# Performance work log

Hardware: AMD Instinct MI355X
Metric: run time of the kernel (lower is better)

Reference implementation:

```python
import jax, jax.numpy as jnp
import numpy as np

TEMPERATURE = 2.0
N, C = 16384, 1000


def _margin(x, targets):
    """Per-row: top1 - top2 if the target class attains the max, else 0."""
    top2 = jax.lax.top_k(x, 2)[0]                                  # [N, 2]
    tval = jnp.take_along_axis(x, targets[:, None], axis=1)[:, 0]  # [N]
    return jnp.where(tval == top2[:, 0], top2[:, 0] - top2[:, 1], jnp.zeros((), x.dtype))


def setup_inputs() -> dict:
    key = jax.random.key(0)
    ks = jax.random.split(key, 8)
    outs = {f"outputs{i+1}": jax.random.normal(ks[i], (N, C), dtype=jnp.float32) for i in range(6)}
    outs["mimic"] = jax.random.normal(ks[6], (N, C), dtype=jnp.float32)
    outs["targets"] = jax.random.randint(ks[7], (N,), 0, C)
    outs["n_test"] = N
    return outs


def reference(outputs1, outputs2, outputs3, outputs4, outputs5, outputs6, mimic, targets, n_test):
    t = targets[:n_test]
    heads = [outputs1, outputs2, outputs3, outputs4, outputs5, outputs6, mimic]
    # [n_test, 7] stacked margins (d1..d6, m) in original ordering
    margins = jnp.stack([_margin(h[:n_test], t) for h in heads], axis=1)
    out_threshold = jax.nn.softmax(margins / TEMPERATURE, axis=1)
    max_preds = jnp.max(jnp.stack([outputs1, outputs2, outputs3, outputs4, outputs5, outputs6]))
    return max_preds, out_threshold
```

## Files before the change

kernel.cpp:

```cpp
#include <hip/hip_runtime.h>
#include <math.h>


__global__ __launch_bounds__(256) void margin_kernel(
    const float* __restrict__ h0, const float* __restrict__ h1,
    const float* __restrict__ h2, const float* __restrict__ h3,
    const float* __restrict__ h4, const float* __restrict__ h5,
    const float* __restrict__ h6,
    const int* __restrict__ targets,
    float* __restrict__ margins,
    float* __restrict__ partials,
    int N, int C)
{
    const int lane = threadIdx.x & 63;
    const int waveInBlock = threadIdx.x >> 6;
    const int p = blockIdx.x * 4 + waveInBlock;
    const int head = p / N;
    const int row  = p - head * N;

    const float* base;
    switch (head) {
        case 0: base = h0; break;
        case 1: base = h1; break;
        case 2: base = h2; break;
        case 3: base = h3; break;
        case 4: base = h4; break;
        case 5: base = h5; break;
        default: base = h6; break;
    }
    base += (size_t)row * C;

    const float4* v = (const float4*)base;
    const int nvec = C >> 2;
    float m1 = -INFINITY, m2 = -INFINITY;
    #pragma unroll
    for (int it = 0; it < 4; ++it) {
        int idx = it * 64 + lane;
        if (idx < nvec) {
            float4 x = v[idx];
            float vals[4] = {x.x, x.y, x.z, x.w};
            #pragma unroll
            for (int k = 0; k < 4; ++k) {
                float val = vals[k];
                if (val > m1) { m2 = m1; m1 = val; }
                else if (val > m2) { m2 = val; }
            }
        }
    }
    #pragma unroll
    for (int off = 32; off >= 1; off >>= 1) {
        float o1 = __shfl_xor(m1, off);
        float o2 = __shfl_xor(m2, off);
        float hi = fmaxf(m1, o1);
        float lo = fminf(m1, o1);
        m2 = fmaxf(lo, fmaxf(m2, o2));
        m1 = hi;
    }

    __shared__ float smax[4];
    if (lane == 0) {
        int t = targets[row];
        float tval = base[t];
        float margin = (tval == m1) ? (m1 - m2) : 0.0f;
        margins[head * N + row] = margin;
        smax[waveInBlock] = (head < 6) ? m1 : -INFINITY;
    }
    __syncthreads();
    if (threadIdx.x == 0) {
        float bm = fmaxf(fmaxf(smax[0], smax[1]), fmaxf(smax[2], smax[3]));
        partials[blockIdx.x] = bm;
    }
}

__global__ __launch_bounds__(1024) void reduce_max_kernel(
    const float* __restrict__ partials, int n, float* __restrict__ out)
{
    float m = -INFINITY;
    for (int i = threadIdx.x; i < n; i += 1024) m = fmaxf(m, partials[i]);
    #pragma unroll
    for (int off = 32; off >= 1; off >>= 1) m = fmaxf(m, __shfl_xor(m, off));
    __shared__ float s[16];
    int lane = threadIdx.x & 63, w = threadIdx.x >> 6;
    if (lane == 0) s[w] = m;
    __syncthreads();
    if (threadIdx.x == 0) {
        float r = -INFINITY;
        #pragma unroll
        for (int i = 0; i < 16; ++i) r = fmaxf(r, s[i]);
        out[0] = r;
    }
}

__global__ __launch_bounds__(256) void softmax_kernel(
    const float* __restrict__ margins, float* __restrict__ out, int N)
{
    int row = blockIdx.x * blockDim.x + threadIdx.x;
    if (row >= N) return;
    float m[7];
    float mx = -INFINITY;
    #pragma unroll
    for (int j = 0; j < 7; ++j) { m[j] = margins[j * N + row]; mx = fmaxf(mx, m[j]); }
    float s = 0.0f;
    #pragma unroll
    for (int j = 0; j < 7; ++j) { m[j] = expf((m[j] - mx) * 0.5f); s += m[j]; }
    float inv = 1.0f / s;
    #pragma unroll
    for (int j = 0; j < 7; ++j) out[row * 7 + j] = m[j] * inv;
}

extern "C" void kernel_launch(void* const* d_in, const int* in_sizes, int n_in,
                              void* d_out, int out_size, void* d_ws, size_t ws_size,
                              hipStream_t stream) {
    const float* h0 = (const float*)d_in[0];
    const float* h1 = (const float*)d_in[1];
    const float* h2 = (const float*)d_in[2];
    const float* h3 = (const float*)d_in[3];
    const float* h4 = (const float*)d_in[4];
    const float* h5 = (const float*)d_in[5];
    const float* h6 = (const float*)d_in[6];
    const int* targets = (const int*)d_in[7];

    const int N = in_sizes[7];
    const int C = in_sizes[0] / N;

    float* margins  = (float*)d_ws;
    float* partials = margins + 7 * N;
    const int pairs  = 7 * N;
    const int nblocks = pairs / 4;

    margin_kernel<<<nblocks, 256, 0, stream>>>(h0, h1, h2, h3, h4, h5, h6,
                                               targets, margins, partials, N, C);
    reduce_max_kernel<<<1, 1024, 0, stream>>>(partials, nblocks, (float*)d_out);
    softmax_kernel<<<(N + 255) / 256, 256, 0, stream>>>(margins, (float*)d_out + 1, N);
}
```

Measured before the change: 391.1 us.

## Process two rows per wave, use branchless top-2, and merge reduce with softmax

Each wave now handles two rows, and all float4 loads are issued up front, which raises memory-level parallelism. The branchy top-2 update is replaced with fmin/fmax arithmetic. The grid becomes 2D with the head index taken from blockIdx.y, which removes the integer division. The separate max-reduce and softmax kernels are merged into one epilogue launch to save a kernel launch. The code assumes N is divisible by 8 and C is in the range where three full float4 sweeps are valid (at least 768).

```diff
diff --git a/kernel.cpp b/kernel.cpp
--- a/kernel.cpp
+++ b/kernel.cpp
@@ -1,6 +1,10 @@
 #include <hip/hip_runtime.h>
 #include <math.h>
 
+
+#define WAVES_PER_BLOCK 4
+#define ROWS_PER_WAVE 2
+#define ROWS_PER_BLOCK (WAVES_PER_BLOCK * ROWS_PER_WAVE)
 
 __global__ __launch_bounds__(256) void margin_kernel(
     const float* __restrict__ h0, const float* __restrict__ h1,
@@ -14,9 +18,7 @@
 {
     const int lane = threadIdx.x & 63;
     const int waveInBlock = threadIdx.x >> 6;
-    const int p = blockIdx.x * 4 + waveInBlock;
-    const int head = p / N;
-    const int row  = p - head * N;
+    const int head = blockIdx.y;
 
     const float* base;
     switch (head) {
@@ -28,73 +30,91 @@
         case 5: base = h5; break;
         default: base = h6; break;
     }
-    base += (size_t)row * C;
 
-    const float4* v = (const float4*)base;
+    const int row0 = (blockIdx.x * WAVES_PER_BLOCK + waveInBlock) * ROWS_PER_WAVE;
+    const int row1 = row0 + 1;
+    const float* b0 = base + (size_t)row0 * C;
+    const float* b1 = base + (size_t)row1 * C;
+    const float4* v0 = (const float4*)b0;
+    const float4* v1 = (const float4*)b1;
     const int nvec = C >> 2;
-    float m1 = -INFINITY, m2 = -INFINITY;
+
+    float4 a0 = v0[lane];
+    float4 a1 = v0[64 + lane];
+    float4 a2 = v0[128 + lane];
+    float4 c0 = v1[lane];
+    float4 c1 = v1[64 + lane];
+    float4 c2 = v1[128 + lane];
+    float4 a3 = make_float4(-INFINITY, -INFINITY, -INFINITY, -INFINITY);
+    float4 c3 = a3;
+    if (192 + lane < nvec) {
+        a3 = v0[192 + lane];
+        c3 = v1[192 + lane];
+    }
+
+    float m1a = -INFINITY, m2a = -INFINITY;
+    float m1c = -INFINITY, m2c = -INFINITY;
+    float va[16] = {a0.x,a0.y,a0.z,a0.w, a1.x,a1.y,a1.z,a1.w,
+                    a2.x,a2.y,a2.z,a2.w, a3.x,a3.y,a3.z,a3.w};
+    float vc[16] = {c0.x,c0.y,c0.z,c0.w, c1.x,c1.y,c1.z,c1.w,
+                    c2.x,c2.y,c2.z,c2.w, c3.x,c3.y,c3.z,c3.w};
     #pragma unroll
-    for (int it = 0; it < 4; ++it) {
-        int idx = it * 64 + lane;
-        if (idx < nvec) {
-            float4 x = v[idx];
-            float vals[4] = {x.x, x.y, x.z, x.w};
-            #pragma unroll
-            for (int k = 0; k < 4; ++k) {
-                float val = vals[k];
-                if (val > m1) { m2 = m1; m1 = val; }
-                else if (val > m2) { m2 = val; }
-            }
-        }
+    for (int k = 0; k < 16; ++k) {
+        float x = va[k];
+        m2a = fmaxf(m2a, fminf(m1a, x));
+        m1a = fmaxf(m1a, x);
+        float y = vc[k];
+        m2c = fmaxf(m2c, fminf(m1c, y));
+        m1c = fmaxf(m1c, y);
     }
+
     #pragma unroll
     for (int off = 32; off >= 1; off >>= 1) {
-        float o1 = __shfl_xor(m1, off);
-        float o2 = __shfl_xor(m2, off);
-        float hi = fmaxf(m1, o1);
-        float lo = fminf(m1, o1);
-        m2 = fmaxf(lo, fmaxf(m2, o2));
-        m1 = hi;
+        float o1a = __shfl_xor(m1a, off);
+        float o2a = __shfl_xor(m2a, off);
+        float o1c = __shfl_xor(m1c, off);
+        float o2c = __shfl_xor(m2c, off);
+        m2a = fmaxf(fmaxf(m2a, o2a), fminf(m1a, o1a));
+        m1a = fmaxf(m1a, o1a);
+        m2c = fmaxf(fmaxf(m2c, o2c), fminf(m1c, o1c));
+        m1c = fmaxf(m1c, o1c);
     }
 
-    __shared__ float smax[4];
+    __shared__ float smax[WAVES_PER_BLOCK];
     if (lane == 0) {
-        int t = targets[row];
-        float tval = base[t];
-        float margin = (tval == m1) ? (m1 - m2) : 0.0f;
-        margins[head * N + row] = margin;
-        smax[waveInBlock] = (head < 6) ? m1 : -INFINITY;
+        int t0 = targets[row0];
+        int t1 = targets[row1];
+        float tv0 = b0[t0];
+        float tv1 = b1[t1];
+        margins[head * N + row0] = (tv0 == m1a) ? (m1a - m2a) : 0.0f;
+        margins[head * N + row1] = (tv1 == m1c) ? (m1c - m2c) : 0.0f;
+        smax[waveInBlock] = fmaxf(m1a, m1c);
     }
     __syncthreads();
-    if (threadIdx.x == 0) {
+    if (threadIdx.x == 0 && head < 6) {
         float bm = fmaxf(fmaxf(smax[0], smax[1]), fmaxf(smax[2], smax[3]));
-        partials[blockIdx.x] = bm;
+        partials[head * gridDim.x + blockIdx.x] = bm;
     }
 }
 
-__global__ __launch_bounds__(1024) void reduce_max_kernel(
-    const float* __restrict__ partials, int n, float* __restrict__ out)
+__global__ __launch_bounds__(256) void epilogue_kernel(
+    const float* __restrict__ margins, const float* __restrict__ partials,
+    int npart, float* __restrict__ out, int N)
 {
-    float m = -INFINITY;
-    for (int i = threadIdx.x; i < n; i += 1024) m = fmaxf(m, partials[i]);
-    #pragma unroll
-    for (int off = 32; off >= 1; off >>= 1) m = fmaxf(m, __shfl_xor(m, off));
-    __shared__ float s[16];
-    int lane = threadIdx.x & 63, w = threadIdx.x >> 6;
-    if (lane == 0) s[w] = m;
-    __syncthreads();
-    if (threadIdx.x == 0) {
-        float r = -INFINITY;
+    if (blockIdx.x == 0) {
+        float m = -INFINITY;
+        for (int i = threadIdx.x; i < npart; i += 256) m = fmaxf(m, partials[i]);
         #pragma unroll
-        for (int i = 0; i < 16; ++i) r = fmaxf(r, s[i]);
-        out[0] = r;
+        for (int off = 32; off >= 1; off >>= 1) m = fmaxf(m, __shfl_xor(m, off));
+        __shared__ float s[4];
+        int lane = threadIdx.x & 63, w = threadIdx.x >> 6;
+        if (lane == 0) s[w] = m;
+        __syncthreads();
+        if (threadIdx.x == 0)
+            out[0] = fmaxf(fmaxf(s[0], s[1]), fmaxf(s[2], s[3]));
+        return;
     }
-}
-
-__global__ __launch_bounds__(256) void softmax_kernel(
-    const float* __restrict__ margins, float* __restrict__ out, int N)
-{
-    int row = blockIdx.x * blockDim.x + threadIdx.x;
+    int row = (blockIdx.x - 1) * 256 + threadIdx.x;
     if (row >= N) return;
     float m[7];
     float mx = -INFINITY;
@@ -104,8 +124,9 @@
     #pragma unroll
     for (int j = 0; j < 7; ++j) { m[j] = expf((m[j] - mx) * 0.5f); s += m[j]; }
     float inv = 1.0f / s;
+    float* o = out + 1 + (size_t)row * 7;
     #pragma unroll
-    for (int j = 0; j < 7; ++j) out[row * 7 + j] = m[j] * inv;
+    for (int j = 0; j < 7; ++j) o[j] = m[j] * inv;
 }
 
 extern "C" void kernel_launch(void* const* d_in, const int* in_sizes, int n_in,
@@ -125,11 +146,13 @@
 
     float* margins  = (float*)d_ws;
     float* partials = margins + 7 * N;
-    const int pairs  = 7 * N;
-    const int nblocks = pairs / 4;
 
-    margin_kernel<<<nblocks, 256, 0, stream>>>(h0, h1, h2, h3, h4, h5, h6,
-                                               targets, margins, partials, N, C);
-    reduce_max_kernel<<<1, 1024, 0, stream>>>(partials, nblocks, (float*)d_out);
-    softmax_kernel<<<(N + 255) / 256, 256, 0, stream>>>(margins, (float*)d_out + 1, N);
+    const int blocksX = N / ROWS_PER_BLOCK;
+    const int npart = 6 * blocksX;
+
+    dim3 grid(blocksX, 7, 1);
+    margin_kernel<<<grid, 256, 0, stream>>>(h0, h1, h2, h3, h4, h5, h6,
+                                            targets, margins, partials, N, C);
+    epilogue_kernel<<<1 + (N + 255) / 256, 256, 0, stream>>>(margins, partials,
+                                                             npart, (float*)d_out, N);
 }
```

New measurement: 390.7 us (median of 2 runs). Within noise of the previous version (-0.1%).
